# Performance work log

Hardware: AMD Instinct MI355X
Metric: run time of the kernel (lower is better)

The kernel has to match this reference:

```python
import jax, jax.numpy as jnp
import numpy as np

N_NODES = 100000
N_EDGES = 640000
N_FEAT = 128


def setup_inputs() -> dict:
    key = jax.random.key(0)
    k1, k2, k3, k4 = jax.random.split(key, 4)
    x = jax.random.normal(k1, (N_NODES, N_FEAT), dtype=jnp.float32)
    edge_index = jax.random.randint(k2, (2, N_EDGES), 0, N_NODES, dtype=jnp.int32)
    # Glorot-ish init for weights
    W_conv = jax.random.normal(k3, (N_FEAT, N_FEAT), dtype=jnp.float32) / np.sqrt(N_FEAT)
    b_conv = jnp.zeros((N_FEAT,), dtype=jnp.float32)
    W_lin = jax.random.normal(k4, (1, N_FEAT), dtype=jnp.float32) / np.sqrt(N_FEAT)
    b_lin = jnp.zeros((1,), dtype=jnp.float32)
    return {"x": x, "edge_index": edge_index, "W_conv": W_conv,
            "b_conv": b_conv, "W_lin": W_lin, "b_lin": b_lin}


def gcn_conv(x, edge_index, W, b):
    # PyG GCNConv: add self-loops, symmetric normalization D^-1/2 (A+I) D^-1/2,
    # linear transform first (no bias in lin), bias added after aggregation.
    N = x.shape[0]
    loop = jnp.arange(N, dtype=edge_index.dtype)
    src = jnp.concatenate([edge_index[0], loop])  # [E+N]
    dst = jnp.concatenate([edge_index[1], loop])  # [E+N]
    deg = jax.ops.segment_sum(jnp.ones_like(dst, dtype=x.dtype), dst, num_segments=N)
    dinv = jnp.where(deg > 0, jax.lax.rsqrt(deg), 0.0)
    norm = dinv[src] * dinv[dst]                   # [E+N]
    xw = x @ W.T                                   # [N, F]
    msg = xw[src] * norm[:, None]                  # [E+N, F] gather + scale
    agg = jax.ops.segment_sum(msg, dst, num_segments=N)  # scatter-add
    return agg + b


def reference(x, edge_index, W_conv, b_conv, W_lin, b_lin):
    h = jax.nn.relu(gcn_conv(x, edge_index, W_conv, b_conv))
    out = jax.nn.sigmoid(h @ W_lin.T + b_lin)
    return (out, h)
```

## Files before the change

### kernel.cpp

```cpp
#include <hip/hip_runtime.h>
#include <hip/hip_bf16.h>

#define NN 100000
#define NE 640000
#define NF 128
#define CAP 32
#define ECAP 36
#define LDW 136
#define EBLK 625
#define XBLK 6250
#define WBLK 8

typedef short bf16x8 __attribute__((ext_vector_type(8)));
typedef float f32x4  __attribute__((ext_vector_type(4)));

__device__ __forceinline__ unsigned short f2bf(float f) {
    union { float f; unsigned int i; } v; v.f = f;
    unsigned int x = v.i;
    return (unsigned short)((x + 0x7FFFu + ((x >> 16) & 1u)) >> 16);
}

__global__ void k_zero(int* __restrict__ fill) {
    int i = blockIdx.x * blockDim.x + threadIdx.x;
    if (i < NN / 4) *(int4*)(fill + i * 4) = (int4){0, 0, 0, 0};
}

__global__ void k_build(const float* __restrict__ x, const float* __restrict__ W,
                        const int* __restrict__ src, const int* __restrict__ dst,
                        int* __restrict__ fill, int* __restrict__ esrc,
                        unsigned short* __restrict__ xs,
                        unsigned short* __restrict__ wb) {
    int b = blockIdx.x;
    if (b < EBLK) {
        int e = (b * 256 + threadIdx.x) * 4;
        int4 s4 = *(const int4*)(src + e);
        int4 d4 = *(const int4*)(dst + e);
        int p0 = atomicAdd(&fill[d4.x], 1);
        int p1 = atomicAdd(&fill[d4.y], 1);
        int p2 = atomicAdd(&fill[d4.z], 1);
        int p3 = atomicAdd(&fill[d4.w], 1);
        if (p0 < CAP) esrc[(long)d4.x * CAP + p0] = s4.x;
        if (p1 < CAP) esrc[(long)d4.y * CAP + p1] = s4.y;
        if (p2 < CAP) esrc[(long)d4.z * CAP + p2] = s4.z;
        if (p3 < CAP) esrc[(long)d4.w * CAP + p3] = s4.w;
    } else if (b < EBLK + XBLK) {
        int t = (b - EBLK) * 256 + threadIdx.x;
        int node = t >> 4, fc = (t & 15) * 8;
        const float* xp = x + (long)node * NF + fc;
        float4 a = *(const float4*)(xp);
        float4 c = *(const float4*)(xp + 4);
        int4 u;
        u.x = (unsigned)f2bf(a.x) | ((unsigned)f2bf(a.y) << 16);
        u.y = (unsigned)f2bf(a.z) | ((unsigned)f2bf(a.w) << 16);
        u.z = (unsigned)f2bf(c.x) | ((unsigned)f2bf(c.y) << 16);
        u.w = (unsigned)f2bf(c.z) | ((unsigned)f2bf(c.w) << 16);
        *(int4*)(xs + (long)node * NF + fc) = u;
    } else {
        int t = (b - EBLK - XBLK) * 256 + threadIdx.x;
        int idx = t * 8;
        float4 a = *(const float4*)(W + idx);
        float4 c = *(const float4*)(W + idx + 4);
        int4 u;
        u.x = (unsigned)f2bf(a.x) | ((unsigned)f2bf(a.y) << 16);
        u.y = (unsigned)f2bf(a.z) | ((unsigned)f2bf(a.w) << 16);
        u.z = (unsigned)f2bf(c.x) | ((unsigned)f2bf(c.y) << 16);
        u.w = (unsigned)f2bf(c.z) | ((unsigned)f2bf(c.w) << 16);
        *(int4*)(wb + idx) = u;
    }
}

__device__ __forceinline__ void acc_row_s(float* acc, int4 u, float s) {
    acc[0] = fmaf(s, __int_as_float((unsigned)u.x << 16), acc[0]);
    acc[1] = fmaf(s, __int_as_float(u.x & 0xffff0000), acc[1]);
    acc[2] = fmaf(s, __int_as_float((unsigned)u.y << 16), acc[2]);
    acc[3] = fmaf(s, __int_as_float(u.y & 0xffff0000), acc[3]);
    acc[4] = fmaf(s, __int_as_float((unsigned)u.z << 16), acc[4]);
    acc[5] = fmaf(s, __int_as_float(u.z & 0xffff0000), acc[5]);
    acc[6] = fmaf(s, __int_as_float((unsigned)u.w << 16), acc[6]);
    acc[7] = fmaf(s, __int_as_float(u.w & 0xffff0000), acc[7]);
}

__launch_bounds__(256, 4)
__global__ void k_fused(const unsigned short* __restrict__ xs,
                        const int* __restrict__ fill,
                        const int* __restrict__ esrc,
                        const unsigned short* __restrict__ wb,
                        const float* __restrict__ bconv,
                        const float* __restrict__ wlin,
                        const float* __restrict__ blin,
                        float* __restrict__ out,
                        float* __restrict__ hout) {
    __shared__ unsigned short lds_a[32 * LDW];
    __shared__ int lds_e[32 * ECAP];
    __shared__ float lds_dv[32];
    __shared__ int lds_dg[32];
    __shared__ float sh_head[2][32];
    int t = threadIdx.x;
    int row0 = blockIdx.x * 32;

    {
        int r = t >> 3, col = (t & 7) * 4;
        *(int4*)(lds_e + r * ECAP + col) =
            *(const int4*)(esrc + (long)(row0 + r) * CAP + col);
    }
    if (t < 32) {
        int dg = fill[row0 + t];
        lds_dv[t] = rsqrtf((float)(dg + 1));
        lds_dg[t] = (dg > CAP) ? CAP : dg;
    }
    __syncthreads();

    {
        int lane = t & 15, slot = t >> 4;
        int fc = lane * 8;
        for (int m = 0; m < 2; ++m) {
            int r = m * 16 + slot;
            int node = row0 + r;
            float dv = lds_dv[r];
            int degc = lds_dg[r];
            const int* ep = lds_e + r * ECAP;

            float acc[8];
            {
                int4 us = *(const int4*)(xs + (long)node * NF + fc);
                acc[0] = dv * __int_as_float((unsigned)us.x << 16);
                acc[1] = dv * __int_as_float(us.x & 0xffff0000);
                acc[2] = dv * __int_as_float((unsigned)us.y << 16);
                acc[3] = dv * __int_as_float(us.y & 0xffff0000);
                acc[4] = dv * __int_as_float((unsigned)us.z << 16);
                acc[5] = dv * __int_as_float(us.z & 0xffff0000);
                acc[6] = dv * __int_as_float((unsigned)us.w << 16);
                acc[7] = dv * __int_as_float(us.w & 0xffff0000);
            }

            for (int j = 0; j < degc; j += 8) {
                int i0 = (j + 0 < degc) ? ep[j + 0] : node;
                int i1 = (j + 1 < degc) ? ep[j + 1] : node;
                int i2 = (j + 2 < degc) ? ep[j + 2] : node;
                int i3 = (j + 3 < degc) ? ep[j + 3] : node;
                int i4 = (j + 4 < degc) ? ep[j + 4] : node;
                int i5 = (j + 5 < degc) ? ep[j + 5] : node;
                int i6 = (j + 6 < degc) ? ep[j + 6] : node;
                int i7 = (j + 7 < degc) ? ep[j + 7] : node;
                int f0 = fill[i0], f1 = fill[i1];
                int f2 = fill[i2], f3 = fill[i3];
                int f4 = fill[i4], f5 = fill[i5];
                int f6 = fill[i6], f7 = fill[i7];
                int4 v0 = *(const int4*)(xs + (long)i0 * NF + fc);
                int4 v1 = *(const int4*)(xs + (long)i1 * NF + fc);
                int4 v2 = *(const int4*)(xs + (long)i2 * NF + fc);
                int4 v3 = *(const int4*)(xs + (long)i3 * NF + fc);
                int4 v4 = *(const int4*)(xs + (long)i4 * NF + fc);
                int4 v5 = *(const int4*)(xs + (long)i5 * NF + fc);
                int4 v6 = *(const int4*)(xs + (long)i6 * NF + fc);
                int4 v7 = *(const int4*)(xs + (long)i7 * NF + fc);
                float s0 = (j + 0 < degc) ? rsqrtf((float)(f0 + 1)) : 0.f;
                float s1 = (j + 1 < degc) ? rsqrtf((float)(f1 + 1)) : 0.f;
                float s2 = (j + 2 < degc) ? rsqrtf((float)(f2 + 1)) : 0.f;
                float s3 = (j + 3 < degc) ? rsqrtf((float)(f3 + 1)) : 0.f;
                float s4 = (j + 4 < degc) ? rsqrtf((float)(f4 + 1)) : 0.f;
                float s5 = (j + 5 < degc) ? rsqrtf((float)(f5 + 1)) : 0.f;
                float s6 = (j + 6 < degc) ? rsqrtf((float)(f6 + 1)) : 0.f;
                float s7 = (j + 7 < degc) ? rsqrtf((float)(f7 + 1)) : 0.f;
                acc_row_s(acc, v0, s0); acc_row_s(acc, v1, s1);
                acc_row_s(acc, v2, s2); acc_row_s(acc, v3, s3);
                acc_row_s(acc, v4, s4); acc_row_s(acc, v5, s5);
                acc_row_s(acc, v6, s6); acc_row_s(acc, v7, s7);
            }

            int4 st;
            st.x = (unsigned)f2bf(acc[0] * dv) | ((unsigned)f2bf(acc[1] * dv) << 16);
            st.y = (unsigned)f2bf(acc[2] * dv) | ((unsigned)f2bf(acc[3] * dv) << 16);
            st.z = (unsigned)f2bf(acc[4] * dv) | ((unsigned)f2bf(acc[5] * dv) << 16);
            st.w = (unsigned)f2bf(acc[6] * dv) | ((unsigned)f2bf(acc[7] * dv) << 16);
            *(int4*)(lds_a + r * LDW + fc) = st;
        }
    }
    __syncthreads();

    int w = t >> 6, lane = t & 63;
    int quad = lane >> 4, nr = lane & 15;
    int mrow = (w >> 1) * 16;
    int ncol0 = (w & 1) * 64;
    int kq = quad * 8;

    f32x4 acc4[4];
#pragma unroll
    for (int nt = 0; nt < 4; ++nt) acc4[nt] = (f32x4){0.f, 0.f, 0.f, 0.f};

#pragma unroll
    for (int ks = 0; ks < 4; ++ks) {
        bf16x8 af = *(const bf16x8*)(lds_a + (mrow + nr) * LDW + ks * 32 + kq);
#pragma unroll
        for (int nt = 0; nt < 4; ++nt) {
            bf16x8 bf = *(const bf16x8*)(wb + (ncol0 + nt * 16 + nr) * NF + ks * 32 + kq);
            acc4[nt] = __builtin_amdgcn_mfma_f32_16x16x32_bf16(af, bf, acc4[nt], 0, 0, 0);
        }
    }

    float bcv[4], wlv[4];
#pragma unroll
    for (int nt = 0; nt < 4; ++nt) {
        int col = ncol0 + nt * 16 + nr;
        bcv[nt] = bconv[col];
        wlv[nt] = wlin[col];
    }
    float p[4] = {0.f, 0.f, 0.f, 0.f};
#pragma unroll
    for (int nt = 0; nt < 4; ++nt) {
        int col = ncol0 + nt * 16 + nr;
#pragma unroll
        for (int r = 0; r < 4; ++r) {
            float h = fmaxf(acc4[nt][r] + bcv[nt], 0.0f);
            int row = row0 + mrow + quad * 4 + r;
            hout[(long)row * NF + col] = h;
            p[r] += h * wlv[nt];
        }
    }
#pragma unroll
    for (int r = 0; r < 4; ++r) {
#pragma unroll
        for (int off = 1; off <= 8; off <<= 1)
            p[r] += __shfl_xor(p[r], off, 64);
        if (nr == 0) sh_head[w & 1][mrow + quad * 4 + r] = p[r];
    }
    __syncthreads();
    if (t < 32) {
        float z = sh_head[0][t] + sh_head[1][t] + blin[0];
        out[row0 + t] = 1.0f / (1.0f + expf(-z));
    }
}

extern "C" void kernel_launch(void* const* d_in, const int* in_sizes, int n_in,
                              void* d_out, int out_size, void* d_ws, size_t ws_size,
                              hipStream_t stream) {
    const float* x     = (const float*)d_in[0];
    const int*   ei    = (const int*)d_in[1];
    const float* Wc    = (const float*)d_in[2];
    const float* bconv = (const float*)d_in[3];
    const float* wlin  = (const float*)d_in[4];
    const float* blin  = (const float*)d_in[5];
    const int* src = ei;
    const int* dst = ei + NE;

    float* out  = (float*)d_out;
    float* hout = out + NN;

    int*            esrc = (int*)d_ws;
    unsigned short* xs   = (unsigned short*)(esrc + (size_t)NN * CAP);
    unsigned short* wb   = xs + (size_t)NN * NF;
    int*            fill = (int*)(wb + NF * NF);

    k_zero <<<(NN / 4 + 255) / 256, 256, 0, stream>>>(fill);
    k_build<<<EBLK + XBLK + WBLK, 256, 0, stream>>>(x, Wc, src, dst,
                                                    fill, esrc, xs, wb);
    k_fused<<<NN / 32, 256, 0, stream>>>(xs, fill, esrc, wb,
                                         bconv, wlin, blin, out, hout);
}
```

Baseline: 200.9 us.

## Restructure fused GCN kernel to per-wave 16-row tiles held in MFMA registers

The fused kernel now gives each wavefront 16 nodes. Each lane gathers and aggregates neighbour features directly into the bf16 A-fragment layout the MFMA expects, so the LDS staging buffers and block-wide barriers are gone. Each wave computes the full 128-column output and the head reduction itself. The edge-build blocks also switch from four edges per thread to one. The cost is more registers per lane (32 accumulators plus 16 in-flight int4 loads), and each lane now serialises over its own node's neighbour list, so degree variance within a wave causes divergence.

```diff
diff --git a/kernel.cpp b/kernel.cpp
--- a/kernel.cpp
+++ b/kernel.cpp
@@ -5,11 +5,10 @@
 #define NE 640000
 #define NF 128
 #define CAP 32
-#define ECAP 36
-#define LDW 136
-#define EBLK 625
+#define EBLK 2500
 #define XBLK 6250
 #define WBLK 8
+#define NWAVE 6250
 
 typedef short bf16x8 __attribute__((ext_vector_type(8)));
 typedef float f32x4  __attribute__((ext_vector_type(4)));
@@ -19,6 +18,8 @@
     unsigned int x = v.i;
     return (unsigned short)((x + 0x7FFFu + ((x >> 16) & 1u)) >> 16);
 }
+__device__ __forceinline__ float bflo(int u) { return __int_as_float((unsigned)u << 16); }
+__device__ __forceinline__ float bfhi(int u) { return __int_as_float(u & 0xffff0000); }
 
 __global__ void k_zero(int* __restrict__ fill) {
     int i = blockIdx.x * blockDim.x + threadIdx.x;
@@ -32,17 +33,10 @@
                         unsigned short* __restrict__ wb) {
     int b = blockIdx.x;
     if (b < EBLK) {
-        int e = (b * 256 + threadIdx.x) * 4;
-        int4 s4 = *(const int4*)(src + e);
-        int4 d4 = *(const int4*)(dst + e);
-        int p0 = atomicAdd(&fill[d4.x], 1);
-        int p1 = atomicAdd(&fill[d4.y], 1);
-        int p2 = atomicAdd(&fill[d4.z], 1);
-        int p3 = atomicAdd(&fill[d4.w], 1);
-        if (p0 < CAP) esrc[(long)d4.x * CAP + p0] = s4.x;
-        if (p1 < CAP) esrc[(long)d4.y * CAP + p1] = s4.y;
-        if (p2 < CAP) esrc[(long)d4.z * CAP + p2] = s4.z;
-        if (p3 < CAP) esrc[(long)d4.w * CAP + p3] = s4.w;
+        int e = b * 256 + threadIdx.x;
+        int s = src[e], d = dst[e];
+        int pos = atomicAdd(&fill[d], 1);
+        if (pos < CAP) esrc[(long)d * CAP + pos] = s;
     } else if (b < EBLK + XBLK) {
         int t = (b - EBLK) * 256 + threadIdx.x;
         int node = t >> 4, fc = (t & 15) * 8;
@@ -69,15 +63,11 @@
     }
 }
 
-__device__ __forceinline__ void acc_row_s(float* acc, int4 u, float s) {
-    acc[0] = fmaf(s, __int_as_float((unsigned)u.x << 16), acc[0]);
-    acc[1] = fmaf(s, __int_as_float(u.x & 0xffff0000), acc[1]);
-    acc[2] = fmaf(s, __int_as_float((unsigned)u.y << 16), acc[2]);
-    acc[3] = fmaf(s, __int_as_float(u.y & 0xffff0000), acc[3]);
-    acc[4] = fmaf(s, __int_as_float((unsigned)u.z << 16), acc[4]);
-    acc[5] = fmaf(s, __int_as_float(u.z & 0xffff0000), acc[5]);
-    acc[6] = fmaf(s, __int_as_float((unsigned)u.w << 16), acc[6]);
-    acc[7] = fmaf(s, __int_as_float(u.w & 0xffff0000), acc[7]);
+__device__ __forceinline__ void acc8(float* a, int4 u, float s) {
+    a[0] = fmaf(s, bflo(u.x), a[0]); a[1] = fmaf(s, bfhi(u.x), a[1]);
+    a[2] = fmaf(s, bflo(u.y), a[2]); a[3] = fmaf(s, bfhi(u.y), a[3]);
+    a[4] = fmaf(s, bflo(u.z), a[4]); a[5] = fmaf(s, bfhi(u.z), a[5]);
+    a[6] = fmaf(s, bflo(u.w), a[6]); a[7] = fmaf(s, bfhi(u.w), a[7]);
 }
 
 __launch_bounds__(256, 4)
@@ -90,144 +80,109 @@
                         const float* __restrict__ blin,
                         float* __restrict__ out,
                         float* __restrict__ hout) {
-    __shared__ unsigned short lds_a[32 * LDW];
-    __shared__ int lds_e[32 * ECAP];
-    __shared__ float lds_dv[32];
-    __shared__ int lds_dg[32];
-    __shared__ float sh_head[2][32];
-    int t = threadIdx.x;
-    int row0 = blockIdx.x * 32;
-
-    {
-        int r = t >> 3, col = (t & 7) * 4;
-        *(int4*)(lds_e + r * ECAP + col) =
-            *(const int4*)(esrc + (long)(row0 + r) * CAP + col);
-    }
-    if (t < 32) {
-        int dg = fill[row0 + t];
-        lds_dv[t] = rsqrtf((float)(dg + 1));
-        lds_dg[t] = (dg > CAP) ? CAP : dg;
-    }
-    __syncthreads();
-
-    {
-        int lane = t & 15, slot = t >> 4;
-        int fc = lane * 8;
-        for (int m = 0; m < 2; ++m) {
-            int r = m * 16 + slot;
-            int node = row0 + r;
-            float dv = lds_dv[r];
-            int degc = lds_dg[r];
-            const int* ep = lds_e + r * ECAP;
-
-            float acc[8];
-            {
-                int4 us = *(const int4*)(xs + (long)node * NF + fc);
-                acc[0] = dv * __int_as_float((unsigned)us.x << 16);
-                acc[1] = dv * __int_as_float(us.x & 0xffff0000);
-                acc[2] = dv * __int_as_float((unsigned)us.y << 16);
-                acc[3] = dv * __int_as_float(us.y & 0xffff0000);
-                acc[4] = dv * __int_as_float((unsigned)us.z << 16);
-                acc[5] = dv * __int_as_float(us.z & 0xffff0000);
-                acc[6] = dv * __int_as_float((unsigned)us.w << 16);
-                acc[7] = dv * __int_as_float(us.w & 0xffff0000);
-            }
-
-            for (int j = 0; j < degc; j += 8) {
-                int i0 = (j + 0 < degc) ? ep[j + 0] : node;
-                int i1 = (j + 1 < degc) ? ep[j + 1] : node;
-                int i2 = (j + 2 < degc) ? ep[j + 2] : node;
-                int i3 = (j + 3 < degc) ? ep[j + 3] : node;
-                int i4 = (j + 4 < degc) ? ep[j + 4] : node;
-                int i5 = (j + 5 < degc) ? ep[j + 5] : node;
-                int i6 = (j + 6 < degc) ? ep[j + 6] : node;
-                int i7 = (j + 7 < degc) ? ep[j + 7] : node;
-                int f0 = fill[i0], f1 = fill[i1];
-                int f2 = fill[i2], f3 = fill[i3];
-                int f4 = fill[i4], f5 = fill[i5];
-                int f6 = fill[i6], f7 = fill[i7];
-                int4 v0 = *(const int4*)(xs + (long)i0 * NF + fc);
-                int4 v1 = *(const int4*)(xs + (long)i1 * NF + fc);
-                int4 v2 = *(const int4*)(xs + (long)i2 * NF + fc);
-                int4 v3 = *(const int4*)(xs + (long)i3 * NF + fc);
-                int4 v4 = *(const int4*)(xs + (long)i4 * NF + fc);
-                int4 v5 = *(const int4*)(xs + (long)i5 * NF + fc);
-                int4 v6 = *(const int4*)(xs + (long)i6 * NF + fc);
-                int4 v7 = *(const int4*)(xs + (long)i7 * NF + fc);
-                float s0 = (j + 0 < degc) ? rsqrtf((float)(f0 + 1)) : 0.f;
-                float s1 = (j + 1 < degc) ? rsqrtf((float)(f1 + 1)) : 0.f;
-                float s2 = (j + 2 < degc) ? rsqrtf((float)(f2 + 1)) : 0.f;
-                float s3 = (j + 3 < degc) ? rsqrtf((float)(f3 + 1)) : 0.f;
-                float s4 = (j + 4 < degc) ? rsqrtf((float)(f4 + 1)) : 0.f;
-                float s5 = (j + 5 < degc) ? rsqrtf((float)(f5 + 1)) : 0.f;
-                float s6 = (j + 6 < degc) ? rsqrtf((float)(f6 + 1)) : 0.f;
-                float s7 = (j + 7 < degc) ? rsqrtf((float)(f7 + 1)) : 0.f;
-                acc_row_s(acc, v0, s0); acc_row_s(acc, v1, s1);
-                acc_row_s(acc, v2, s2); acc_row_s(acc, v3, s3);
-                acc_row_s(acc, v4, s4); acc_row_s(acc, v5, s5);
-                acc_row_s(acc, v6, s6); acc_row_s(acc, v7, s7);
-            }
-
-            int4 st;
-            st.x = (unsigned)f2bf(acc[0] * dv) | ((unsigned)f2bf(acc[1] * dv) << 16);
-            st.y = (unsigned)f2bf(acc[2] * dv) | ((unsigned)f2bf(acc[3] * dv) << 16);
-            st.z = (unsigned)f2bf(acc[4] * dv) | ((unsigned)f2bf(acc[5] * dv) << 16);
-            st.w = (unsigned)f2bf(acc[6] * dv) | ((unsigned)f2bf(acc[7] * dv) << 16);
-            *(int4*)(lds_a + r * LDW + fc) = st;
+    int wv = blockIdx.x * 4 + (threadIdx.x >> 6);
+    if (wv >= NWAVE) return;
+    int row0 = wv * 16;
+    int l = threadIdx.x & 63;
+    int r = l & 15, q = l >> 4;
+    int node = row0 + r;
+    int kq = q * 8;
+
+    int deg = fill[node];
+    float dv = rsqrtf((float)(deg + 1));
+    int degc = (deg > CAP) ? CAP : deg;
+    const unsigned short* xrow = xs + (long)node * NF + kq;
+
+    float acc[4][8];
+#pragma unroll
+    for (int ks = 0; ks < 4; ++ks) {
+        int4 u = *(const int4*)(xrow + ks * 32);
+        acc[ks][0] = dv * bflo(u.x); acc[ks][1] = dv * bfhi(u.x);
+        acc[ks][2] = dv * bflo(u.y); acc[ks][3] = dv * bfhi(u.y);
+        acc[ks][4] = dv * bflo(u.z); acc[ks][5] = dv * bfhi(u.z);
+        acc[ks][6] = dv * bflo(u.w); acc[ks][7] = dv * bfhi(u.w);
+    }
+
+    const int* ep = esrc + (long)node * CAP;
+    for (int j = 0; j < degc; j += 4) {
+        int4 e4 = *(const int4*)(ep + j);
+        int i0 = (j + 0 < degc) ? e4.x : node;
+        int i1 = (j + 1 < degc) ? e4.y : node;
+        int i2 = (j + 2 < degc) ? e4.z : node;
+        int i3 = (j + 3 < degc) ? e4.w : node;
+        int f0 = fill[i0], f1 = fill[i1], f2 = fill[i2], f3 = fill[i3];
+        const unsigned short* p0 = xs + (long)i0 * NF + kq;
+        const unsigned short* p1 = xs + (long)i1 * NF + kq;
+        const unsigned short* p2 = xs + (long)i2 * NF + kq;
+        const unsigned short* p3 = xs + (long)i3 * NF + kq;
+        int4 v00 = *(const int4*)(p0);       int4 v01 = *(const int4*)(p0 + 32);
+        int4 v02 = *(const int4*)(p0 + 64);  int4 v03 = *(const int4*)(p0 + 96);
+        int4 v10 = *(const int4*)(p1);       int4 v11 = *(const int4*)(p1 + 32);
+        int4 v12 = *(const int4*)(p1 + 64);  int4 v13 = *(const int4*)(p1 + 96);
+        int4 v20 = *(const int4*)(p2);       int4 v21 = *(const int4*)(p2 + 32);
+        int4 v22 = *(const int4*)(p2 + 64);  int4 v23 = *(const int4*)(p2 + 96);
+        int4 v30 = *(const int4*)(p3);       int4 v31 = *(const int4*)(p3 + 32);
+        int4 v32 = *(const int4*)(p3 + 64);  int4 v33 = *(const int4*)(p3 + 96);
+        float s0 = (j + 0 < degc) ? rsqrtf((float)(f0 + 1)) : 0.f;
+        float s1 = (j + 1 < degc) ? rsqrtf((float)(f1 + 1)) : 0.f;
+        float s2 = (j + 2 < degc) ? rsqrtf((float)(f2 + 1)) : 0.f;
+        float s3 = (j + 3 < degc) ? rsqrtf((float)(f3 + 1)) : 0.f;
+        acc8(acc[0], v00, s0); acc8(acc[1], v01, s0);
+        acc8(acc[2], v02, s0); acc8(acc[3], v03, s0);
+        acc8(acc[0], v10, s1); acc8(acc[1], v11, s1);
+        acc8(acc[2], v12, s1); acc8(acc[3], v13, s1);
+        acc8(acc[0], v20, s2); acc8(acc[1], v21, s2);
+        acc8(acc[2], v22, s2); acc8(acc[3], v23, s2);
+        acc8(acc[0], v30, s3); acc8(acc[1], v31, s3);
+        acc8(acc[2], v32, s3); acc8(acc[3], v33, s3);
+    }
+
+    bf16x8 af[4];
+#pragma unroll
+    for (int ks = 0; ks < 4; ++ks) {
+#pragma unroll
+        for (int e = 0; e < 8; ++e)
+            af[ks][e] = (short)f2bf(acc[ks][e] * dv);
+    }
+
+    f32x4 c[8];
+#pragma unroll
+    for (int nt = 0; nt < 8; ++nt) c[nt] = (f32x4){0.f, 0.f, 0.f, 0.f};
+#pragma unroll
+    for (int nt = 0; nt < 8; ++nt) {
+        const unsigned short* wrow = wb + (nt * 16 + r) * NF + kq;
+#pragma unroll
+        for (int ks = 0; ks < 4; ++ks) {
+            bf16x8 bfr = *(const bf16x8*)(wrow + ks * 32);
+            c[nt] = __builtin_amdgcn_mfma_f32_16x16x32_bf16(af[ks], bfr, c[nt], 0, 0, 0);
         }
     }
-    __syncthreads();
-
-    int w = t >> 6, lane = t & 63;
-    int quad = lane >> 4, nr = lane & 15;
-    int mrow = (w >> 1) * 16;
-    int ncol0 = (w & 1) * 64;
-    int kq = quad * 8;
-
-    f32x4 acc4[4];
-#pragma unroll
-    for (int nt = 0; nt < 4; ++nt) acc4[nt] = (f32x4){0.f, 0.f, 0.f, 0.f};
-
-#pragma unroll
-    for (int ks = 0; ks < 4; ++ks) {
-        bf16x8 af = *(const bf16x8*)(lds_a + (mrow + nr) * LDW + ks * 32 + kq);
-#pragma unroll
-        for (int nt = 0; nt < 4; ++nt) {
-            bf16x8 bf = *(const bf16x8*)(wb + (ncol0 + nt * 16 + nr) * NF + ks * 32 + kq);
-            acc4[nt] = __builtin_amdgcn_mfma_f32_16x16x32_bf16(af, bf, acc4[nt], 0, 0, 0);
+
+    float p[4] = {0.f, 0.f, 0.f, 0.f};
+#pragma unroll
+    for (int nt = 0; nt < 8; ++nt) {
+        int col = nt * 16 + r;
+        float bc = bconv[col], wl = wlin[col];
+#pragma unroll
+        for (int g = 0; g < 4; ++g) {
+            float h = fmaxf(c[nt][g] + bc, 0.f);
+            hout[(long)(row0 + q * 4 + g) * NF + col] = h;
+            p[g] = fmaf(h, wl, p[g]);
         }
     }
-
-    float bcv[4], wlv[4];
-#pragma unroll
-    for (int nt = 0; nt < 4; ++nt) {
-        int col = ncol0 + nt * 16 + nr;
-        bcv[nt] = bconv[col];
-        wlv[nt] = wlin[col];
-    }
-    float p[4] = {0.f, 0.f, 0.f, 0.f};
-#pragma unroll
-    for (int nt = 0; nt < 4; ++nt) {
-        int col = ncol0 + nt * 16 + nr;
-#pragma unroll
-        for (int r = 0; r < 4; ++r) {
-            float h = fmaxf(acc4[nt][r] + bcv[nt], 0.0f);
-            int row = row0 + mrow + quad * 4 + r;
-            hout[(long)row * NF + col] = h;
-            p[r] += h * wlv[nt];
+#pragma unroll
+    for (int g = 0; g < 4; ++g) {
+#pragma unroll
+        for (int off = 1; off <= 8; off <<= 1)
+            p[g] += __shfl_xor(p[g], off, 64);
+    }
+    if (r == 0) {
+        float bl = blin[0];
+#pragma unroll
+        for (int g = 0; g < 4; ++g) {
+            float z = p[g] + bl;
+            out[row0 + q * 4 + g] = 1.0f / (1.0f + expf(-z));
         }
-    }
-#pragma unroll
-    for (int r = 0; r < 4; ++r) {
-#pragma unroll
-        for (int off = 1; off <= 8; off <<= 1)
-            p[r] += __shfl_xor(p[r], off, 64);
-        if (nr == 0) sh_head[w & 1][mrow + quad * 4 + r] = p[r];
-    }
-    __syncthreads();
-    if (t < 32) {
-        float z = sh_head[0][t] + sh_head[1][t] + blin[0];
-        out[row0 + t] = 1.0f / (1.0f + expf(-z));
     }
 }
 
@@ -254,6 +209,6 @@
     k_zero <<<(NN / 4 + 255) / 256, 256, 0, stream>>>(fill);
     k_build<<<EBLK + XBLK + WBLK, 256, 0, stream>>>(x, Wc, src, dst,
                                                     fill, esrc, xs, wb);
-    k_fused<<<NN / 32, 256, 0, stream>>>(xs, fill, esrc, wb,
-                                         bconv, wlin, blin, out, hout);
-}
+    k_fused<<<(NWAVE + 3) / 4, 256, 0, stream>>>(xs, fill, esrc, wb,
+                                                 bconv, wlin, blin, out, hout);
+}
```

Result: slower. 260.4 us (+29.6%).

## Merge build and fused kernels into persistent kernel with grid barrier and tile queue

Applied to the files above, without the earlier changes.

The edge-bucketing/bf16-conversion kernel and the aggregation+MFMA kernel are merged into one persistent kernel of 1280 blocks. A software grid barrier built on atomics separates the two phases, and tiles are handed out through an atomic work counter. The aim is to remove a kernel launch boundary and the tail effects between phases. The cost is a spin-wait barrier that assumes all 1280 blocks are co-resident (risk of deadlock otherwise), plus per-tile atomic and sync overhead. The edge phase also loses the 4-wide vectorized loads.

```diff
diff --git a/kernel.cpp b/kernel.cpp
--- a/kernel.cpp
+++ b/kernel.cpp
@@ -7,9 +7,11 @@
 #define CAP 32
 #define ECAP 36
 #define LDW 136
-#define EBLK 625
-#define XBLK 6250
-#define WBLK 8
+#define NB 1280
+#define EBLKS 512
+#define CBLKS (NB - EBLKS)
+#define NTILE 3125
+#define NN_PAD 100352
 
 typedef short bf16x8 __attribute__((ext_vector_type(8)));
 typedef float f32x4  __attribute__((ext_vector_type(4)));
@@ -19,215 +21,226 @@
     unsigned int x = v.i;
     return (unsigned short)((x + 0x7FFFu + ((x >> 16) & 1u)) >> 16);
 }
-
-__global__ void k_zero(int* __restrict__ fill) {
+__device__ __forceinline__ float bflo(int u) { return __int_as_float((unsigned)u << 16); }
+__device__ __forceinline__ float bfhi(int u) { return __int_as_float(u & 0xffff0000); }
+
+__global__ void k_init(int* __restrict__ fill, int* __restrict__ ctrl) {
     int i = blockIdx.x * blockDim.x + threadIdx.x;
-    if (i < NN / 4) *(int4*)(fill + i * 4) = (int4){0, 0, 0, 0};
-}
-
-__global__ void k_build(const float* __restrict__ x, const float* __restrict__ W,
-                        const int* __restrict__ src, const int* __restrict__ dst,
-                        int* __restrict__ fill, int* __restrict__ esrc,
-                        unsigned short* __restrict__ xs,
-                        unsigned short* __restrict__ wb) {
-    int b = blockIdx.x;
-    if (b < EBLK) {
-        int e = (b * 256 + threadIdx.x) * 4;
-        int4 s4 = *(const int4*)(src + e);
-        int4 d4 = *(const int4*)(dst + e);
-        int p0 = atomicAdd(&fill[d4.x], 1);
-        int p1 = atomicAdd(&fill[d4.y], 1);
-        int p2 = atomicAdd(&fill[d4.z], 1);
-        int p3 = atomicAdd(&fill[d4.w], 1);
-        if (p0 < CAP) esrc[(long)d4.x * CAP + p0] = s4.x;
-        if (p1 < CAP) esrc[(long)d4.y * CAP + p1] = s4.y;
-        if (p2 < CAP) esrc[(long)d4.z * CAP + p2] = s4.z;
-        if (p3 < CAP) esrc[(long)d4.w * CAP + p3] = s4.w;
-    } else if (b < EBLK + XBLK) {
-        int t = (b - EBLK) * 256 + threadIdx.x;
-        int node = t >> 4, fc = (t & 15) * 8;
-        const float* xp = x + (long)node * NF + fc;
-        float4 a = *(const float4*)(xp);
-        float4 c = *(const float4*)(xp + 4);
-        int4 u;
-        u.x = (unsigned)f2bf(a.x) | ((unsigned)f2bf(a.y) << 16);
-        u.y = (unsigned)f2bf(a.z) | ((unsigned)f2bf(a.w) << 16);
-        u.z = (unsigned)f2bf(c.x) | ((unsigned)f2bf(c.y) << 16);
-        u.w = (unsigned)f2bf(c.z) | ((unsigned)f2bf(c.w) << 16);
-        *(int4*)(xs + (long)node * NF + fc) = u;
-    } else {
-        int t = (b - EBLK - XBLK) * 256 + threadIdx.x;
-        int idx = t * 8;
-        float4 a = *(const float4*)(W + idx);
-        float4 c = *(const float4*)(W + idx + 4);
-        int4 u;
-        u.x = (unsigned)f2bf(a.x) | ((unsigned)f2bf(a.y) << 16);
-        u.y = (unsigned)f2bf(a.z) | ((unsigned)f2bf(a.w) << 16);
-        u.z = (unsigned)f2bf(c.x) | ((unsigned)f2bf(c.y) << 16);
-        u.w = (unsigned)f2bf(c.z) | ((unsigned)f2bf(c.w) << 16);
-        *(int4*)(wb + idx) = u;
+    if (i < NN_PAD / 4) *(int4*)(fill + i * 4) = (int4){0, 0, 0, 0};
+    if (i < 4) ctrl[i] = 0;
+}
+
+__device__ __forceinline__ void gridbar(int* __restrict__ cnt, int* __restrict__ gen) {
+    __syncthreads();
+    if (threadIdx.x == 0) {
+        __threadfence();
+        int g = __hip_atomic_load(gen, __ATOMIC_SEQ_CST, __HIP_MEMORY_SCOPE_AGENT);
+        int a = __hip_atomic_fetch_add(cnt, 1, __ATOMIC_SEQ_CST, __HIP_MEMORY_SCOPE_AGENT);
+        if (a == NB - 1) {
+            __hip_atomic_store(cnt, 0, __ATOMIC_RELAXED, __HIP_MEMORY_SCOPE_AGENT);
+            __hip_atomic_store(gen, g + 1, __ATOMIC_SEQ_CST, __HIP_MEMORY_SCOPE_AGENT);
+        } else {
+            while (__hip_atomic_load(gen, __ATOMIC_SEQ_CST, __HIP_MEMORY_SCOPE_AGENT) == g)
+                __builtin_amdgcn_s_sleep(2);
+        }
+        __threadfence();
     }
+    __syncthreads();
 }
 
 __device__ __forceinline__ void acc_row_s(float* acc, int4 u, float s) {
-    acc[0] = fmaf(s, __int_as_float((unsigned)u.x << 16), acc[0]);
-    acc[1] = fmaf(s, __int_as_float(u.x & 0xffff0000), acc[1]);
-    acc[2] = fmaf(s, __int_as_float((unsigned)u.y << 16), acc[2]);
-    acc[3] = fmaf(s, __int_as_float(u.y & 0xffff0000), acc[3]);
-    acc[4] = fmaf(s, __int_as_float((unsigned)u.z << 16), acc[4]);
-    acc[5] = fmaf(s, __int_as_float(u.z & 0xffff0000), acc[5]);
-    acc[6] = fmaf(s, __int_as_float((unsigned)u.w << 16), acc[6]);
-    acc[7] = fmaf(s, __int_as_float(u.w & 0xffff0000), acc[7]);
-}
-
-__launch_bounds__(256, 4)
-__global__ void k_fused(const unsigned short* __restrict__ xs,
-                        const int* __restrict__ fill,
-                        const int* __restrict__ esrc,
-                        const unsigned short* __restrict__ wb,
-                        const float* __restrict__ bconv,
-                        const float* __restrict__ wlin,
-                        const float* __restrict__ blin,
-                        float* __restrict__ out,
-                        float* __restrict__ hout) {
+    acc[0] = fmaf(s, bflo(u.x), acc[0]); acc[1] = fmaf(s, bfhi(u.x), acc[1]);
+    acc[2] = fmaf(s, bflo(u.y), acc[2]); acc[3] = fmaf(s, bfhi(u.y), acc[3]);
+    acc[4] = fmaf(s, bflo(u.z), acc[4]); acc[5] = fmaf(s, bfhi(u.z), acc[5]);
+    acc[6] = fmaf(s, bflo(u.w), acc[6]); acc[7] = fmaf(s, bfhi(u.w), acc[7]);
+}
+
+__launch_bounds__(256, 6)
+__global__ void k_mega(const float* __restrict__ x, const float* __restrict__ W,
+                       const int* __restrict__ src, const int* __restrict__ dst,
+                       int* __restrict__ fill, int* __restrict__ esrc,
+                       unsigned short* __restrict__ xs, unsigned short* __restrict__ wb,
+                       const float* __restrict__ bconv, const float* __restrict__ wlin,
+                       const float* __restrict__ blin,
+                       float* __restrict__ out, float* __restrict__ hout,
+                       int* __restrict__ ctrl) {
     __shared__ unsigned short lds_a[32 * LDW];
     __shared__ int lds_e[32 * ECAP];
     __shared__ float lds_dv[32];
     __shared__ int lds_dg[32];
     __shared__ float sh_head[2][32];
-    int t = threadIdx.x;
-    int row0 = blockIdx.x * 32;
-
-    {
-        int r = t >> 3, col = (t & 7) * 4;
-        *(int4*)(lds_e + r * ECAP + col) =
-            *(const int4*)(esrc + (long)(row0 + r) * CAP + col);
+    __shared__ int sh_tile;
+    int bid = blockIdx.x, t = threadIdx.x;
+
+    if (bid < EBLKS) {
+        for (int e = bid * 256 + t; e < NE; e += EBLKS * 256) {
+            int s = src[e], d = dst[e];
+            int pos = atomicAdd(&fill[d], 1);
+            if (pos < CAP) esrc[(long)d * CAP + pos] = s;
+        }
+    } else {
+        for (int ct = (bid - EBLKS) * 256 + t; ct < NN * 16; ct += CBLKS * 256) {
+            int node = ct >> 4, fc = (ct & 15) * 8;
+            const float* xp = x + (long)node * NF + fc;
+            float4 a = *(const float4*)(xp);
+            float4 c = *(const float4*)(xp + 4);
+            int4 u;
+            u.x = (unsigned)f2bf(a.x) | ((unsigned)f2bf(a.y) << 16);
+            u.y = (unsigned)f2bf(a.z) | ((unsigned)f2bf(a.w) << 16);
+            u.z = (unsigned)f2bf(c.x) | ((unsigned)f2bf(c.y) << 16);
+            u.w = (unsigned)f2bf(c.z) | ((unsigned)f2bf(c.w) << 16);
+            *(int4*)(xs + (long)node * NF + fc) = u;
+        }
+        if (bid == EBLKS) {
+            for (int ct = t; ct < 2048; ct += 256) {
+                int idx = ct * 8;
+                float4 a = *(const float4*)(W + idx);
+                float4 c = *(const float4*)(W + idx + 4);
+                int4 u;
+                u.x = (unsigned)f2bf(a.x) | ((unsigned)f2bf(a.y) << 16);
+                u.y = (unsigned)f2bf(a.z) | ((unsigned)f2bf(a.w) << 16);
+                u.z = (unsigned)f2bf(c.x) | ((unsigned)f2bf(c.y) << 16);
+                u.w = (unsigned)f2bf(c.z) | ((unsigned)f2bf(c.w) << 16);
+                *(int4*)(wb + idx) = u;
+            }
+        }
     }
-    if (t < 32) {
-        int dg = fill[row0 + t];
-        lds_dv[t] = rsqrtf((float)(dg + 1));
-        lds_dg[t] = (dg > CAP) ? CAP : dg;
-    }
-    __syncthreads();
-
-    {
-        int lane = t & 15, slot = t >> 4;
-        int fc = lane * 8;
-        for (int m = 0; m < 2; ++m) {
-            int r = m * 16 + slot;
-            int node = row0 + r;
-            float dv = lds_dv[r];
-            int degc = lds_dg[r];
-            const int* ep = lds_e + r * ECAP;
-
-            float acc[8];
-            {
-                int4 us = *(const int4*)(xs + (long)node * NF + fc);
-                acc[0] = dv * __int_as_float((unsigned)us.x << 16);
-                acc[1] = dv * __int_as_float(us.x & 0xffff0000);
-                acc[2] = dv * __int_as_float((unsigned)us.y << 16);
-                acc[3] = dv * __int_as_float(us.y & 0xffff0000);
-                acc[4] = dv * __int_as_float((unsigned)us.z << 16);
-                acc[5] = dv * __int_as_float(us.z & 0xffff0000);
-                acc[6] = dv * __int_as_float((unsigned)us.w << 16);
-                acc[7] = dv * __int_as_float(us.w & 0xffff0000);
-            }
-
-            for (int j = 0; j < degc; j += 8) {
-                int i0 = (j + 0 < degc) ? ep[j + 0] : node;
-                int i1 = (j + 1 < degc) ? ep[j + 1] : node;
-                int i2 = (j + 2 < degc) ? ep[j + 2] : node;
-                int i3 = (j + 3 < degc) ? ep[j + 3] : node;
-                int i4 = (j + 4 < degc) ? ep[j + 4] : node;
-                int i5 = (j + 5 < degc) ? ep[j + 5] : node;
-                int i6 = (j + 6 < degc) ? ep[j + 6] : node;
-                int i7 = (j + 7 < degc) ? ep[j + 7] : node;
-                int f0 = fill[i0], f1 = fill[i1];
-                int f2 = fill[i2], f3 = fill[i3];
-                int f4 = fill[i4], f5 = fill[i5];
-                int f6 = fill[i6], f7 = fill[i7];
-                int4 v0 = *(const int4*)(xs + (long)i0 * NF + fc);
-                int4 v1 = *(const int4*)(xs + (long)i1 * NF + fc);
-                int4 v2 = *(const int4*)(xs + (long)i2 * NF + fc);
-                int4 v3 = *(const int4*)(xs + (long)i3 * NF + fc);
-                int4 v4 = *(const int4*)(xs + (long)i4 * NF + fc);
-                int4 v5 = *(const int4*)(xs + (long)i5 * NF + fc);
-                int4 v6 = *(const int4*)(xs + (long)i6 * NF + fc);
-                int4 v7 = *(const int4*)(xs + (long)i7 * NF + fc);
-                float s0 = (j + 0 < degc) ? rsqrtf((float)(f0 + 1)) : 0.f;
-                float s1 = (j + 1 < degc) ? rsqrtf((float)(f1 + 1)) : 0.f;
-                float s2 = (j + 2 < degc) ? rsqrtf((float)(f2 + 1)) : 0.f;
-                float s3 = (j + 3 < degc) ? rsqrtf((float)(f3 + 1)) : 0.f;
-                float s4 = (j + 4 < degc) ? rsqrtf((float)(f4 + 1)) : 0.f;
-                float s5 = (j + 5 < degc) ? rsqrtf((float)(f5 + 1)) : 0.f;
-                float s6 = (j + 6 < degc) ? rsqrtf((float)(f6 + 1)) : 0.f;
-                float s7 = (j + 7 < degc) ? rsqrtf((float)(f7 + 1)) : 0.f;
-                acc_row_s(acc, v0, s0); acc_row_s(acc, v1, s1);
-                acc_row_s(acc, v2, s2); acc_row_s(acc, v3, s3);
-                acc_row_s(acc, v4, s4); acc_row_s(acc, v5, s5);
-                acc_row_s(acc, v6, s6); acc_row_s(acc, v7, s7);
-            }
-
-            int4 st;
-            st.x = (unsigned)f2bf(acc[0] * dv) | ((unsigned)f2bf(acc[1] * dv) << 16);
-            st.y = (unsigned)f2bf(acc[2] * dv) | ((unsigned)f2bf(acc[3] * dv) << 16);
-            st.z = (unsigned)f2bf(acc[4] * dv) | ((unsigned)f2bf(acc[5] * dv) << 16);
-            st.w = (unsigned)f2bf(acc[6] * dv) | ((unsigned)f2bf(acc[7] * dv) << 16);
-            *(int4*)(lds_a + r * LDW + fc) = st;
-        }
-    }
-    __syncthreads();
-
-    int w = t >> 6, lane = t & 63;
-    int quad = lane >> 4, nr = lane & 15;
-    int mrow = (w >> 1) * 16;
-    int ncol0 = (w & 1) * 64;
-    int kq = quad * 8;
-
-    f32x4 acc4[4];
-#pragma unroll
-    for (int nt = 0; nt < 4; ++nt) acc4[nt] = (f32x4){0.f, 0.f, 0.f, 0.f};
-
-#pragma unroll
-    for (int ks = 0; ks < 4; ++ks) {
-        bf16x8 af = *(const bf16x8*)(lds_a + (mrow + nr) * LDW + ks * 32 + kq);
+
+    gridbar(ctrl + 1, ctrl + 2);
+
+    for (;;) {
+        if (t == 0) sh_tile = atomicAdd(&ctrl[0], 1);
+        __syncthreads();
+        int tile = sh_tile;
+        if (tile >= NTILE) break;
+        int row0 = tile * 32;
+
+        {
+            int r = t >> 3, col = (t & 7) * 4;
+            *(int4*)(lds_e + r * ECAP + col) =
+                *(const int4*)(esrc + (long)(row0 + r) * CAP + col);
+        }
+        if (t < 32) {
+            int dg = fill[row0 + t];
+            lds_dv[t] = rsqrtf((float)(dg + 1));
+            lds_dg[t] = (dg > CAP) ? CAP : dg;
+        }
+        __syncthreads();
+
+        {
+            int lane = t & 15, slot = t >> 4;
+            int fc = lane * 8;
+            for (int m = 0; m < 2; ++m) {
+                int r = m * 16 + slot;
+                int node = row0 + r;
+                float dv = lds_dv[r];
+                int degc = lds_dg[r];
+                const int* ep = lds_e + r * ECAP;
+
+                float acc[8];
+                {
+                    int4 us = *(const int4*)(xs + (long)node * NF + fc);
+                    acc[0] = dv * bflo(us.x); acc[1] = dv * bfhi(us.x);
+                    acc[2] = dv * bflo(us.y); acc[3] = dv * bfhi(us.y);
+                    acc[4] = dv * bflo(us.z); acc[5] = dv * bfhi(us.z);
+                    acc[6] = dv * bflo(us.w); acc[7] = dv * bfhi(us.w);
+                }
+                for (int j = 0; j < degc; j += 8) {
+                    int i0 = (j + 0 < degc) ? ep[j + 0] : node;
+                    int i1 = (j + 1 < degc) ? ep[j + 1] : node;
+                    int i2 = (j + 2 < degc) ? ep[j + 2] : node;
+                    int i3 = (j + 3 < degc) ? ep[j + 3] : node;
+                    int i4 = (j + 4 < degc) ? ep[j + 4] : node;
+                    int i5 = (j + 5 < degc) ? ep[j + 5] : node;
+                    int i6 = (j + 6 < degc) ? ep[j + 6] : node;
+                    int i7 = (j + 7 < degc) ? ep[j + 7] : node;
+                    int f0 = fill[i0], f1 = fill[i1];
+                    int f2 = fill[i2], f3 = fill[i3];
+                    int f4 = fill[i4], f5 = fill[i5];
+                    int f6 = fill[i6], f7 = fill[i7];
+                    int4 v0 = *(const int4*)(xs + (long)i0 * NF + fc);
+                    int4 v1 = *(const int4*)(xs + (long)i1 * NF + fc);
+                    int4 v2 = *(const int4*)(xs + (long)i2 * NF + fc);
+                    int4 v3 = *(const int4*)(xs + (long)i3 * NF + fc);
+                    int4 v4 = *(const int4*)(xs + (long)i4 * NF + fc);
+                    int4 v5 = *(const int4*)(xs + (long)i5 * NF + fc);
+                    int4 v6 = *(const int4*)(xs + (long)i6 * NF + fc);
+                    int4 v7 = *(const int4*)(xs + (long)i7 * NF + fc);
+                    float s0 = (j + 0 < degc) ? rsqrtf((float)(f0 + 1)) : 0.f;
+                    float s1 = (j + 1 < degc) ? rsqrtf((float)(f1 + 1)) : 0.f;
+                    float s2 = (j + 2 < degc) ? rsqrtf((float)(f2 + 1)) : 0.f;
+                    float s3 = (j + 3 < degc) ? rsqrtf((float)(f3 + 1)) : 0.f;
+                    float s4 = (j + 4 < degc) ? rsqrtf((float)(f4 + 1)) : 0.f;
+                    float s5 = (j + 5 < degc) ? rsqrtf((float)(f5 + 1)) : 0.f;
+                    float s6 = (j + 6 < degc) ? rsqrtf((float)(f6 + 1)) : 0.f;
+                    float s7 = (j + 7 < degc) ? rsqrtf((float)(f7 + 1)) : 0.f;
+                    acc_row_s(acc, v0, s0); acc_row_s(acc, v1, s1);
+                    acc_row_s(acc, v2, s2); acc_row_s(acc, v3, s3);
+                    acc_row_s(acc, v4, s4); acc_row_s(acc, v5, s5);
+                    acc_row_s(acc, v6, s6); acc_row_s(acc, v7, s7);
+                }
+
+                int4 st;
+                st.x = (unsigned)f2bf(acc[0] * dv) | ((unsigned)f2bf(acc[1] * dv) << 16);
+                st.y = (unsigned)f2bf(acc[2] * dv) | ((unsigned)f2bf(acc[3] * dv) << 16);
+                st.z = (unsigned)f2bf(acc[4] * dv) | ((unsigned)f2bf(acc[5] * dv) << 16);
+                st.w = (unsigned)f2bf(acc[6] * dv) | ((unsigned)f2bf(acc[7] * dv) << 16);
+                *(int4*)(lds_a + r * LDW + fc) = st;
+            }
+        }
+        __syncthreads();
+
+        int w = t >> 6, lane = t & 63;
+        int quad = lane >> 4, nr = lane & 15;
+        int mrow = (w >> 1) * 16;
+        int ncol0 = (w & 1) * 64;
+        int kq = quad * 8;
+
+        f32x4 acc4[4];
+#pragma unroll
+        for (int nt = 0; nt < 4; ++nt) acc4[nt] = (f32x4){0.f, 0.f, 0.f, 0.f};
+#pragma unroll
+        for (int ks = 0; ks < 4; ++ks) {
+            bf16x8 af = *(const bf16x8*)(lds_a + (mrow + nr) * LDW + ks * 32 + kq);
+#pragma unroll
+            for (int nt = 0; nt < 4; ++nt) {
+                bf16x8 bfr = *(const bf16x8*)(wb + (ncol0 + nt * 16 + nr) * NF + ks * 32 + kq);
+                acc4[nt] = __builtin_amdgcn_mfma_f32_16x16x32_bf16(af, bfr, acc4[nt], 0, 0, 0);
+            }
+        }
+
+        float bcv[4], wlv[4];
 #pragma unroll
         for (int nt = 0; nt < 4; ++nt) {
-            bf16x8 bf = *(const bf16x8*)(wb + (ncol0 + nt * 16 + nr) * NF + ks * 32 + kq);
-            acc4[nt] = __builtin_amdgcn_mfma_f32_16x16x32_bf16(af, bf, acc4[nt], 0, 0, 0);
-        }
-    }
-
-    float bcv[4], wlv[4];
-#pragma unroll
-    for (int nt = 0; nt < 4; ++nt) {
-        int col = ncol0 + nt * 16 + nr;
-        bcv[nt] = bconv[col];
-        wlv[nt] = wlin[col];
-    }
-    float p[4] = {0.f, 0.f, 0.f, 0.f};
-#pragma unroll
-    for (int nt = 0; nt < 4; ++nt) {
-        int col = ncol0 + nt * 16 + nr;
+            int col = ncol0 + nt * 16 + nr;
+            bcv[nt] = bconv[col];
+            wlv[nt] = wlin[col];
+        }
+        float p[4] = {0.f, 0.f, 0.f, 0.f};
+#pragma unroll
+        for (int nt = 0; nt < 4; ++nt) {
+            int col = ncol0 + nt * 16 + nr;
+#pragma unroll
+            for (int r = 0; r < 4; ++r) {
+                float h = fmaxf(acc4[nt][r] + bcv[nt], 0.0f);
+                int row = row0 + mrow + quad * 4 + r;
+                hout[(long)row * NF + col] = h;
+                p[r] += h * wlv[nt];
+            }
+        }
 #pragma unroll
         for (int r = 0; r < 4; ++r) {
-            float h = fmaxf(acc4[nt][r] + bcv[nt], 0.0f);
-            int row = row0 + mrow + quad * 4 + r;
-            hout[(long)row * NF + col] = h;
-            p[r] += h * wlv[nt];
-        }
-    }
-#pragma unroll
-    for (int r = 0; r < 4; ++r) {
-#pragma unroll
-        for (int off = 1; off <= 8; off <<= 1)
-            p[r] += __shfl_xor(p[r], off, 64);
-        if (nr == 0) sh_head[w & 1][mrow + quad * 4 + r] = p[r];
-    }
-    __syncthreads();
-    if (t < 32) {
-        float z = sh_head[0][t] + sh_head[1][t] + blin[0];
-        out[row0 + t] = 1.0f / (1.0f + expf(-z));
+#pragma unroll
+            for (int off = 1; off <= 8; off <<= 1)
+                p[r] += __shfl_xor(p[r], off, 64);
+            if (nr == 0) sh_head[w & 1][mrow + quad * 4 + r] = p[r];
+        }
+        __syncthreads();
+        if (t < 32) {
+            float z = sh_head[0][t] + sh_head[1][t] + blin[0];
+            out[row0 + t] = 1.0f / (1.0f + expf(-z));
+        }
+        __syncthreads();
     }
 }
 
@@ -250,10 +263,9 @@
     unsigned short* xs   = (unsigned short*)(esrc + (size_t)NN * CAP);
     unsigned short* wb   = xs + (size_t)NN * NF;
     int*            fill = (int*)(wb + NF * NF);
-
-    k_zero <<<(NN / 4 + 255) / 256, 256, 0, stream>>>(fill);
-    k_build<<<EBLK + XBLK + WBLK, 256, 0, stream>>>(x, Wc, src, dst,
-                                                    fill, esrc, xs, wb);
-    k_fused<<<NN / 32, 256, 0, stream>>>(xs, fill, esrc, wb,
-                                         bconv, wlin, blin, out, hout);
-}
+    int*            ctrl = fill + NN_PAD;
+
+    k_init<<<(NN_PAD / 4 + 255) / 256, 256, 0, stream>>>(fill, ctrl);
+    k_mega<<<NB, 256, 0, stream>>>(x, Wc, src, dst, fill, esrc, xs, wb,
+                                   bconv, wlin, blin, out, hout, ctrl);
+}
```

After: 533.2 us. +165.4%, slower.
